# Kernel optimization log

Hardware: AMD Instinct MI355X
Metric: run time of the kernel (lower is better)

The kernel has to match this reference:

```python
import jax, jax.numpy as jnp
import numpy as np

B, C, N = 8, 512, 2048

def setup_inputs() -> dict:
    key = jax.random.key(0)
    ks = jax.random.split(key, 7)
    s = 1.0 / np.sqrt(C)
    return {
        "x": jax.random.normal(ks[0], (B, C, N), dtype=jnp.float32),
        "wq": jax.random.normal(ks[1], (C, C), dtype=jnp.float32) * s,
        "bq": jax.random.normal(ks[2], (C,), dtype=jnp.float32) * s,
        "wk": jax.random.normal(ks[3], (C, C), dtype=jnp.float32) * s,
        "bk": jax.random.normal(ks[4], (C,), dtype=jnp.float32) * s,
        "wv": jax.random.normal(ks[5], (C, C), dtype=jnp.float32) * s,
        "bv": jax.random.normal(ks[6], (C,), dtype=jnp.float32) * s,
    }

def reference(x, wq, bq, wk, bk, wv, bv):
    # Conv1d with kernel=1 == pointwise channel matmul: [B,C,N] -> [B,C,N]
    q = jnp.einsum('oc,bcn->bon', wq, x) + bq[None, :, None]
    k = jnp.einsum('oc,bcn->bon', wk, x) + bk[None, :, None]
    v = jnp.einsum('oc,bcn->bon', wv, x) + bv[None, :, None]
    # scores[b,i,j] = sum_c q[b,c,i] * k[b,c,j]; softmax over j (no scaling, as in source)
    scores = jnp.einsum('bci,bcj->bij', q, k)
    attn = jax.nn.softmax(scores, axis=-1)  # [B,N,N]
    # out[b,c,i] = sum_j v[b,c,j] * attn[b,i,j]
    out = jnp.einsum('bcj,bij->bci', v, attn)
    return out + x
```

## Files before the change

### kernel.cpp

```cpp
#include <hip/hip_runtime.h>
#include <hip/hip_bf16.h>

typedef _Float16 half_t;
typedef _Float16 f16x8 __attribute__((ext_vector_type(8)));
typedef float f32x4 __attribute__((ext_vector_type(4)));

#define AS1 __attribute__((address_space(1)))
#define AS3 __attribute__((address_space(3)))

constexpr int CB = 512;
constexpr int NB = 2048;
constexpr int BB = 8;

__device__ inline f32x4 mfma16(f16x8 a, f16x8 b, f32x4 c) {
  return __builtin_amdgcn_mfma_f32_16x16x32_f16(a, b, c, 0, 0, 0);
}

__device__ inline void xcd_swizzle(int& bx, int& by, int& bz) {
  const int gx = gridDim.x, gy = gridDim.y, gz = gridDim.z;
  const int nwg = gx * gy * gz;
  int lin = blockIdx.x + gx * (blockIdx.y + gy * blockIdx.z);
  if ((nwg & 7) == 0) {
    const int q = nwg >> 3;
    lin = (lin & 7) * q + (lin >> 3);
  }
  bx = lin % gx;
  int tmp = lin / gx;
  by = tmp % gy;
  bz = tmp / gy;
}

__global__ void prep_wu(const float* __restrict__ wv, const float* __restrict__ wk,
                        const float* __restrict__ bq,
                        half_t* __restrict__ wvh, float* __restrict__ u) {
  if (blockIdx.x < 1024) {
    int i = blockIdx.x * 256 + threadIdx.x;
    if (i < CB * CB) wvh[i] = (half_t)wv[i];
  } else {
    int d = (blockIdx.x - 1024) * 256 + threadIdx.x;
    if (d < CB) {
      float s = 0.0f;
      for (int o = 0; o < CB; o++) s += bq[o] * wk[(size_t)o * CB + d];
      u[d] = s;
    }
  }
}

__global__ __launch_bounds__(256) void compute_G_part(const float* __restrict__ wq,
                                                      const float* __restrict__ wk,
                                                      float* __restrict__ Gp) {
  __shared__ float aq[64][68];
  __shared__ float ak[64][68];
  const int c0 = blockIdx.y * 64, d0 = blockIdx.x * 64, o0 = blockIdx.z * 64;
  const int t = threadIdx.x;
  {
    const int r = t >> 2, cbase = (t & 3) * 16;
    const float* q = wq + (size_t)(o0 + r) * CB + c0 + cbase;
    const float* k = wk + (size_t)(o0 + r) * CB + d0 + cbase;
#pragma unroll
    for (int q4 = 0; q4 < 4; q4++) {
      *(float4*)&aq[r][cbase + q4 * 4] = *(const float4*)(q + q4 * 4);
      *(float4*)&ak[r][cbase + q4 * 4] = *(const float4*)(k + q4 * 4);
    }
  }
  __syncthreads();
  const int tc = t & 15, td = t >> 4;
  float acc[4][4] = {};
#pragma unroll 8
  for (int o = 0; o < 64; o++) {
    float4 a4 = *(const float4*)&aq[o][tc * 4];
    float4 b4 = *(const float4*)&ak[o][td * 4];
    float av[4] = {a4.x, a4.y, a4.z, a4.w};
    float bv[4] = {b4.x, b4.y, b4.z, b4.w};
#pragma unroll
    for (int i = 0; i < 4; i++)
#pragma unroll
      for (int j = 0; j < 4; j++)
        acc[i][j] += av[i] * bv[j];
  }
  float* gz = Gp + (size_t)blockIdx.z * CB * CB;
#pragma unroll
  for (int i = 0; i < 4; i++) {
    int c = c0 + tc * 4 + i;
#pragma unroll
    for (int j = 0; j < 4; j++)
      gz[(size_t)c * CB + d0 + td * 4 + j] = acc[i][j];
  }
}

__global__ void reduce_G(const float* __restrict__ Gp, half_t* __restrict__ Gh) {
  int i = blockIdx.x * 256 + threadIdx.x;
  if (i >= CB * CB) return;
  float s = 0.0f;
#pragma unroll
  for (int z = 0; z < 8; z++) s += Gp[(size_t)z * CB * CB + i];
  Gh[i] = (half_t)s;
}

__global__ __launch_bounds__(256) void compute_ubias(const half_t* __restrict__ xh,
                                                     const float* __restrict__ u,
                                                     float* __restrict__ ub) {
  __shared__ float us[CB];
  for (int i = threadIdx.x; i < CB; i += 256) us[i] = u[i];
  __syncthreads();
  int row = blockIdx.x * 4 + (threadIdx.x >> 6);
  int lane = threadIdx.x & 63;
  f16x8 vh = *(const f16x8*)(xh + (size_t)row * CB + lane * 8);
  float s = 0.0f;
#pragma unroll
  for (int i = 0; i < 8; i++) s += us[lane * 8 + i] * (float)vh[i];
#pragma unroll
  for (int off = 32; off; off >>= 1) s += __shfl_xor(s, off);
  if (lane == 0) ub[row] = s;
}

__global__ void transpose_x(const float* __restrict__ x, half_t* __restrict__ oh,
                            half_t* __restrict__ xn) {
  __shared__ float tile[32][33];
  int b = blockIdx.z, c0 = blockIdx.y * 32, n0 = blockIdx.x * 32;
  int tx = threadIdx.x, ty = threadIdx.y;
  const float* xb = x + (size_t)b * CB * NB;
  half_t* xnb = xn + (size_t)b * CB * NB;
#pragma unroll
  for (int r = 0; r < 4; r++) {
    float v = xb[(size_t)(c0 + ty + 8 * r) * NB + n0 + tx];
    tile[ty + 8 * r][tx] = v;
    xnb[(size_t)(c0 + ty + 8 * r) * NB + n0 + tx] = (half_t)v;
  }
  __syncthreads();
  size_t base = (size_t)b * NB * CB;
#pragma unroll
  for (int r = 0; r < 4; r++)
    oh[base + (size_t)(n0 + ty + 8 * r) * CB + c0 + tx] = (half_t)tile[tx][ty + 8 * r];
}

template <int BIAS, int EPI, int NT>
__global__ __launch_bounds__(256) void gemm_nt(
    const half_t* __restrict__ A, int lda, long sA,
    const half_t* __restrict__ Bh, int ldb, long sB,
    void* __restrict__ D, int ldd, long sD,
    const float* __restrict__ bias, long sBias,
    const half_t* __restrict__ R, int ldr, long sR) {
  constexpr int TSZ = 128 * 32;
  __shared__ alignas(16) half_t sm[3 * 2 * TSZ];

  int bxi, byi, bzi;
  xcd_swizzle(bxi, byi, bzi);
  const int t = threadIdx.x;
  const int z = bzi;
  const half_t* Ab  = A  + (size_t)z * sA + (size_t)(byi * 128) * lda;
  const half_t* Bbh = Bh + (size_t)z * sB + (size_t)(bxi * 128) * ldb;
  const int wid = t >> 6, l15 = t & 15, hi = (t >> 4) & 3;
  const int wr = wid >> 1, wc = wid & 1;
  const int lineA = t >> 2, eoff = (t & 3) * 8;

  f32x4 acc[4][4] = {};

  auto stage = [&](int buf, int kt) {
    half_t* base = sm + buf * (2 * TSZ);
#pragma unroll
    for (int p = 0; p < 2; p++) {
      size_t goA = (size_t)(p * 64 + lineA) * lda + kt * 32 + eoff;
      size_t goB = (size_t)(p * 64 + lineA) * ldb + kt * 32 + eoff;
      int lo = p * 2048 + t * 8;
      __builtin_amdgcn_global_load_lds((const AS1 void*)(Ab + goA),  (AS3 void*)(base + lo), 16, 0, 0);
      __builtin_amdgcn_global_load_lds((const AS1 void*)(Bbh + goB), (AS3 void*)(base + TSZ + lo), 16, 0, 0);
    }
  };

  stage(0, 0);
  stage(1, 1);
  asm volatile("s_waitcnt vmcnt(4)" ::: "memory");
  __builtin_amdgcn_s_barrier();
  asm volatile("" ::: "memory");

  int rb = 0;
  for (int kt = 0; kt < NT; kt++) {
    if (kt + 2 < NT) {
      int sb = rb + 2; if (sb >= 3) sb -= 3;
      stage(sb, kt + 2);
    }
    const half_t* bb = sm + rb * (2 * TSZ);
    f16x8 af[4], bf[4];
#pragma unroll
    for (int f = 0; f < 4; f++) {
      af[f] = *(const f16x8*)(bb + (wr * 64 + f * 16 + l15) * 32 + hi * 8);
      bf[f] = *(const f16x8*)(bb + TSZ + (wc * 64 + f * 16 + l15) * 32 + hi * 8);
    }
#pragma unroll
    for (int fm = 0; fm < 4; fm++)
#pragma unroll
      for (int fn = 0; fn < 4; fn++)
        acc[fm][fn] = mfma16(af[fm], bf[fn], acc[fm][fn]);

    if (kt + 1 < NT) {
      if (kt + 2 < NT) asm volatile("s_waitcnt vmcnt(4)" ::: "memory");
      else             asm volatile("s_waitcnt vmcnt(0)" ::: "memory");
      __builtin_amdgcn_s_barrier();
      asm volatile("" ::: "memory");
    }
    rb = (rb + 1 == 3) ? 0 : rb + 1;
  }

  const int row0 = byi * 128 + wr * 64;
  const int col0 = bxi * 128 + wc * 64;
#pragma unroll
  for (int fm = 0; fm < 4; fm++) {
    int rowb = row0 + fm * 16 + hi * 4;
#pragma unroll
    for (int fn = 0; fn < 4; fn++) {
      int col = col0 + fn * 16 + l15;
      float bc = (BIAS == 1) ? bias[(size_t)z * sBias + col] : 0.0f;
#pragma unroll
      for (int r = 0; r < 4; r++) {
        float val = acc[fm][fn][r] + bc;
        size_t di = (size_t)(rowb + r) * ldd + col;
        if (EPI == 3) {
          val += (float)R[(size_t)z * sR + (size_t)(rowb + r) * ldr + col];
          ((float*)D)[(size_t)z * sD + di] = val;
        } else {
          float sv = fminf(fmaxf(val * 256.0f, -32767.0f), 32767.0f);
          ((short*)D)[(size_t)z * sD + di] = (short)__float2int_rn(sv);
        }
      }
    }
  }
}

__global__ __launch_bounds__(256) void gemm_vyt(
    const half_t* __restrict__ xh, const half_t* __restrict__ wvh,
    const half_t* __restrict__ Gh, const float* __restrict__ bv,
    half_t* __restrict__ v, half_t* __restrict__ YTh) {
  constexpr int TSZ = 128 * 32;
  __shared__ alignas(16) half_t sm[2 * 2 * TSZ];

  int bxi, byi, bzi;
  xcd_swizzle(bxi, byi, bzi);
  const int t = threadIdx.x;

  const half_t* Ab;
  const half_t* Bb;
  half_t* Dz;
  int ldd, row0b, col0b;
  const float* rowbias = nullptr;
  if (bzi < 8) {
    const int z = bzi;
    Ab = wvh + (size_t)(byi * 128) * CB;
    Bb = xh + (size_t)z * NB * CB + (size_t)(bxi * 128) * CB;
    Dz = v + (size_t)z * CB * NB;
    ldd = NB; row0b = byi * 128; col0b = bxi * 128;
    rowbias = bv;
  } else {
    const int z = bzi - 8;
    const int lin2 = byi * 16 + bxi;
    const int xp = lin2 & 3, yp = lin2 >> 2;
    Ab = xh + (size_t)z * NB * CB + (size_t)(yp * 128) * CB;
    Bb = Gh + (size_t)(xp * 128) * CB;
    Dz = YTh + (size_t)z * NB * CB;
    ldd = CB; row0b = yp * 128; col0b = xp * 128;
  }

  const int wid = t >> 6, l15 = t & 15, hi = (t >> 4) & 3;
  const int wr = wid >> 1, wc = wid & 1;
  const int lineA = t >> 2, eoff = (t & 3) * 8;

  f32x4 acc[4][4] = {};

  auto stage = [&](int buf, int kt) {
    half_t* base = sm + buf * (2 * TSZ);
#pragma unroll
    for (int p = 0; p < 2; p++) {
      size_t go = (size_t)(p * 64 + lineA) * CB + kt * 32 + eoff;
      int lo = p * 2048 + t * 8;
      __builtin_amdgcn_global_load_lds((const AS1 void*)(Ab + go), (AS3 void*)(base + lo), 16, 0, 0);
      __builtin_amdgcn_global_load_lds((const AS1 void*)(Bb + go), (AS3 void*)(base + TSZ + lo), 16, 0, 0);
    }
  };

  stage(0, 0);
  __syncthreads();
  int cur = 0;
  for (int kt = 0; kt < 16; kt++) {
    if (kt + 1 < 16) stage(cur ^ 1, kt + 1);
    const half_t* bb = sm + cur * (2 * TSZ);
    f16x8 af[4], bf[4];
#pragma unroll
    for (int f = 0; f < 4; f++) {
      af[f] = *(const f16x8*)(bb + (wr * 64 + f * 16 + l15) * 32 + hi * 8);
      bf[f] = *(const f16x8*)(bb + TSZ + (wc * 64 + f * 16 + l15) * 32 + hi * 8);
    }
#pragma unroll
    for (int fm = 0; fm < 4; fm++)
#pragma unroll
      for (int fn = 0; fn < 4; fn++)
        acc[fm][fn] = mfma16(af[fm], bf[fn], acc[fm][fn]);
    __syncthreads();
    cur ^= 1;
  }

  const int row0 = row0b + wr * 64;
  const int col0 = col0b + wc * 64;
#pragma unroll
  for (int fm = 0; fm < 4; fm++) {
    int rowb = row0 + fm * 16 + hi * 4;
#pragma unroll
    for (int fn = 0; fn < 4; fn++) {
      int col = col0 + fn * 16 + l15;
#pragma unroll
      for (int r = 0; r < 4; r++) {
        float val = acc[fm][fn][r];
        if (rowbias) val += rowbias[rowb + r];
        Dz[(size_t)(rowb + r) * ldd + col] = (half_t)val;
      }
    }
  }
}

struct alignas(16) H8 { half_t h[8]; };
struct alignas(16) S8 { short s[8]; };

__global__ __launch_bounds__(256) void softmax_rows(const short* __restrict__ S,
                                                    half_t* __restrict__ P) {
  const short* row = S + (size_t)blockIdx.x * NB;
  int t = threadIdx.x;
  S8 r8 = *reinterpret_cast<const S8*>(row + t * 8);
  float vals[8];
#pragma unroll
  for (int i = 0; i < 8; i++) vals[i] = (float)r8.s[i] * 0.00390625f;
  float m = vals[0];
#pragma unroll
  for (int i = 1; i < 8; i++) m = fmaxf(m, vals[i]);
#pragma unroll
  for (int off = 32; off; off >>= 1) m = fmaxf(m, __shfl_xor(m, off));
  __shared__ float redm[4], reds[4];
  if ((t & 63) == 0) redm[t >> 6] = m;
  __syncthreads();
  m = fmaxf(fmaxf(redm[0], redm[1]), fmaxf(redm[2], redm[3]));
  float e[8], s = 0.0f;
#pragma unroll
  for (int i = 0; i < 8; i++) { e[i] = __expf(vals[i] - m); s += e[i]; }
#pragma unroll
  for (int off = 32; off; off >>= 1) s += __shfl_xor(s, off);
  if ((t & 63) == 0) reds[t >> 6] = s;
  __syncthreads();
  s = reds[0] + reds[1] + reds[2] + reds[3];
  float inv = 1.0f / s;
  H8 ob;
#pragma unroll
  for (int i = 0; i < 8; i++) ob.h[i] = (half_t)(e[i] * inv);
  *reinterpret_cast<H8*>(P + (size_t)blockIdx.x * NB + t * 8) = ob;
}

extern "C" void kernel_launch(void* const* d_in, const int* in_sizes, int n_in,
                              void* d_out, int out_size, void* d_ws, size_t ws_size,
                              hipStream_t stream) {
  const float* x  = (const float*)d_in[0];
  const float* wq = (const float*)d_in[1];
  const float* bq = (const float*)d_in[2];
  const float* wk = (const float*)d_in[3];
  const float* wv = (const float*)d_in[5];
  const float* bv = (const float*)d_in[6];
  float* out = (float*)d_out;

  const size_t MB = 1u << 20;
  if (ws_size < 196 * MB) return;

  char* ws = (char*)d_ws;
  half_t* xh   = (half_t*)(ws + 0);
  half_t* YTh  = (half_t*)(ws + 16 * MB);
  half_t* v    = (half_t*)(ws + 32 * MB);
  short*  Ss   = (short*)(ws + 48 * MB);
  float*  Gp   = (float*)(ws + 48 * MB);
  half_t* Pd   = (half_t*)(ws + 112 * MB);
  half_t* xn   = (half_t*)(ws + 176 * MB);
  half_t* Gh   = (half_t*)(ws + 192 * MB);
  half_t* wvh  = (half_t*)(ws + 192 * MB + 512 * 1024);
  float*  u    = (float*)(ws + 193 * MB);
  float*  ub   = (float*)(ws + 193 * MB + 256 * 1024);

  prep_wu<<<1026, 256, 0, stream>>>(wv, wk, bq, wvh, u);
  compute_G_part<<<dim3(8, 8, 8), 256, 0, stream>>>(wq, wk, Gp);
  reduce_G<<<1024, 256, 0, stream>>>(Gp, Gh);
  transpose_x<<<dim3(64, 16, 8), dim3(32, 8), 0, stream>>>(x, xh, xn);
  compute_ubias<<<BB * NB / 4, 256, 0, stream>>>(xh, u, ub);

  gemm_vyt<<<dim3(16, 4, 16), 256, 0, stream>>>(xh, wvh, Gh, bv, v, YTh);

  gemm_nt<1, 4, 16><<<dim3(16, 16, 8), 256, 0, stream>>>(
      xh, CB, (long)NB * CB,
      YTh, CB, (long)NB * CB,
      Ss, NB, (long)NB * NB, ub, NB, nullptr, 0, 0);

  softmax_rows<<<BB * NB, 256, 0, stream>>>(Ss, Pd);

  gemm_nt<0, 3, 64><<<dim3(16, 4, 8), 256, 0, stream>>>(
      v, NB, (long)CB * NB,
      Pd, NB, (long)NB * NB,
      out, NB, (long)CB * NB, nullptr, 0,
      xn, NB, (long)CB * NB);
}
```

Measured before the change: 209.5 us.

## Merge prep kernels into two launches and simplify gemm to double buffering

Five small preprocessing kernels (x transpose/convert, partial G, wv conversion, u, G reduction, ubias) are folded into two launches by dispatching on block index, cutting launch count and gaps between dependent kernels. Separately, the gemm_nt main loop goes from a three-stage LDS pipeline with fine-grained vmcnt waits to a two-buffer scheme with a full __syncthreads per iteration. This lowers LDS use per block, which may allow more resident blocks, but it exposes more global-load latency because only one tile is prefetched ahead and every iteration waits for all loads.

```diff
diff --git a/kernel.cpp b/kernel.cpp
--- a/kernel.cpp
+++ b/kernel.cpp
@@ -30,108 +30,116 @@
   bz = tmp / gy;
 }
 
-__global__ void prep_wu(const float* __restrict__ wv, const float* __restrict__ wk,
-                        const float* __restrict__ bq,
-                        half_t* __restrict__ wvh, float* __restrict__ u) {
-  if (blockIdx.x < 1024) {
-    int i = blockIdx.x * 256 + threadIdx.x;
-    if (i < CB * CB) wvh[i] = (half_t)wv[i];
+__global__ __launch_bounds__(256) void prep_all(
+    const float* __restrict__ x, const float* __restrict__ wq,
+    const float* __restrict__ wk, const float* __restrict__ wv,
+    const float* __restrict__ bq,
+    half_t* __restrict__ xh, half_t* __restrict__ xn,
+    half_t* __restrict__ wvh, float* __restrict__ u, float* __restrict__ Gp) {
+  __shared__ float smem[64 * 68 * 2];
+  const int b = blockIdx.x;
+  const int t = threadIdx.x;
+
+  if (b < 8192) {
+    float (*tile)[33] = (float(*)[33])smem;
+    const int bz = b >> 10, by = (b >> 6) & 15, bx = b & 63;
+    const int c0 = by * 32, n0 = bx * 32;
+    const int tx = t & 31, ty = t >> 5;
+    const float* xb = x + (size_t)bz * CB * NB;
+    half_t* xnb = xn + (size_t)bz * CB * NB;
+#pragma unroll
+    for (int r = 0; r < 4; r++) {
+      float v = xb[(size_t)(c0 + ty + 8 * r) * NB + n0 + tx];
+      tile[ty + 8 * r][tx] = v;
+      xnb[(size_t)(c0 + ty + 8 * r) * NB + n0 + tx] = (half_t)v;
+    }
+    __syncthreads();
+    size_t base = (size_t)bz * NB * CB;
+#pragma unroll
+    for (int r = 0; r < 4; r++)
+      xh[base + (size_t)(n0 + ty + 8 * r) * CB + c0 + tx] = (half_t)tile[tx][ty + 8 * r];
+  } else if (b < 8704) {
+    const int g = b - 8192;
+    const int d0 = (g & 7) * 64, c0 = ((g >> 3) & 7) * 64, o0 = (g >> 6) * 64;
+    float (*aq)[68] = (float(*)[68])smem;
+    float (*ak)[68] = (float(*)[68])(smem + 64 * 68);
+    {
+      const int r = t >> 2, cbase = (t & 3) * 16;
+      const float* q = wq + (size_t)(o0 + r) * CB + c0 + cbase;
+      const float* k = wk + (size_t)(o0 + r) * CB + d0 + cbase;
+#pragma unroll
+      for (int q4 = 0; q4 < 4; q4++) {
+        *(float4*)&aq[r][cbase + q4 * 4] = *(const float4*)(q + q4 * 4);
+        *(float4*)&ak[r][cbase + q4 * 4] = *(const float4*)(k + q4 * 4);
+      }
+    }
+    __syncthreads();
+    const int tc = t & 15, td = t >> 4;
+    float acc[4][4] = {};
+#pragma unroll 8
+    for (int o = 0; o < 64; o++) {
+      float4 a4 = *(const float4*)&aq[o][tc * 4];
+      float4 b4 = *(const float4*)&ak[o][td * 4];
+      float av[4] = {a4.x, a4.y, a4.z, a4.w};
+      float bv[4] = {b4.x, b4.y, b4.z, b4.w};
+#pragma unroll
+      for (int i = 0; i < 4; i++)
+#pragma unroll
+        for (int j = 0; j < 4; j++)
+          acc[i][j] += av[i] * bv[j];
+    }
+    float* gz = Gp + (size_t)(g >> 6) * CB * CB;
+#pragma unroll
+    for (int i = 0; i < 4; i++) {
+      int c = c0 + tc * 4 + i;
+#pragma unroll
+      for (int j = 0; j < 4; j++)
+        gz[(size_t)c * CB + d0 + td * 4 + j] = acc[i][j];
+    }
   } else {
-    int d = (blockIdx.x - 1024) * 256 + threadIdx.x;
-    if (d < CB) {
+    const int p = b - 8704;
+    if (p < 1024) {
+      int i = p * 256 + t;
+      if (i < CB * CB) wvh[i] = (half_t)wv[i];
+    } else {
+      int d = (p - 1024) * 256 + t;
+      if (d < CB) {
+        float s = 0.0f;
+        for (int o = 0; o < CB; o++) s += bq[o] * wk[(size_t)o * CB + d];
+        u[d] = s;
+      }
+    }
+  }
+}
+
+__global__ __launch_bounds__(256) void prep2(
+    const float* __restrict__ Gp, half_t* __restrict__ Gh,
+    const half_t* __restrict__ xh, const float* __restrict__ u,
+    float* __restrict__ ub) {
+  const int b = blockIdx.x;
+  const int t = threadIdx.x;
+  if (b < 1024) {
+    int i = b * 256 + t;
+    if (i < CB * CB) {
       float s = 0.0f;
-      for (int o = 0; o < CB; o++) s += bq[o] * wk[(size_t)o * CB + d];
-      u[d] = s;
-    }
-  }
-}
-
-__global__ __launch_bounds__(256) void compute_G_part(const float* __restrict__ wq,
-                                                      const float* __restrict__ wk,
-                                                      float* __restrict__ Gp) {
-  __shared__ float aq[64][68];
-  __shared__ float ak[64][68];
-  const int c0 = blockIdx.y * 64, d0 = blockIdx.x * 64, o0 = blockIdx.z * 64;
-  const int t = threadIdx.x;
-  {
-    const int r = t >> 2, cbase = (t & 3) * 16;
-    const float* q = wq + (size_t)(o0 + r) * CB + c0 + cbase;
-    const float* k = wk + (size_t)(o0 + r) * CB + d0 + cbase;
-#pragma unroll
-    for (int q4 = 0; q4 < 4; q4++) {
-      *(float4*)&aq[r][cbase + q4 * 4] = *(const float4*)(q + q4 * 4);
-      *(float4*)&ak[r][cbase + q4 * 4] = *(const float4*)(k + q4 * 4);
-    }
-  }
-  __syncthreads();
-  const int tc = t & 15, td = t >> 4;
-  float acc[4][4] = {};
-#pragma unroll 8
-  for (int o = 0; o < 64; o++) {
-    float4 a4 = *(const float4*)&aq[o][tc * 4];
-    float4 b4 = *(const float4*)&ak[o][td * 4];
-    float av[4] = {a4.x, a4.y, a4.z, a4.w};
-    float bv[4] = {b4.x, b4.y, b4.z, b4.w};
-#pragma unroll
-    for (int i = 0; i < 4; i++)
-#pragma unroll
-      for (int j = 0; j < 4; j++)
-        acc[i][j] += av[i] * bv[j];
-  }
-  float* gz = Gp + (size_t)blockIdx.z * CB * CB;
-#pragma unroll
-  for (int i = 0; i < 4; i++) {
-    int c = c0 + tc * 4 + i;
-#pragma unroll
-    for (int j = 0; j < 4; j++)
-      gz[(size_t)c * CB + d0 + td * 4 + j] = acc[i][j];
-  }
-}
-
-__global__ void reduce_G(const float* __restrict__ Gp, half_t* __restrict__ Gh) {
-  int i = blockIdx.x * 256 + threadIdx.x;
-  if (i >= CB * CB) return;
-  float s = 0.0f;
-#pragma unroll
-  for (int z = 0; z < 8; z++) s += Gp[(size_t)z * CB * CB + i];
-  Gh[i] = (half_t)s;
-}
-
-__global__ __launch_bounds__(256) void compute_ubias(const half_t* __restrict__ xh,
-                                                     const float* __restrict__ u,
-                                                     float* __restrict__ ub) {
-  __shared__ float us[CB];
-  for (int i = threadIdx.x; i < CB; i += 256) us[i] = u[i];
-  __syncthreads();
-  int row = blockIdx.x * 4 + (threadIdx.x >> 6);
-  int lane = threadIdx.x & 63;
-  f16x8 vh = *(const f16x8*)(xh + (size_t)row * CB + lane * 8);
-  float s = 0.0f;
-#pragma unroll
-  for (int i = 0; i < 8; i++) s += us[lane * 8 + i] * (float)vh[i];
-#pragma unroll
-  for (int off = 32; off; off >>= 1) s += __shfl_xor(s, off);
-  if (lane == 0) ub[row] = s;
-}
-
-__global__ void transpose_x(const float* __restrict__ x, half_t* __restrict__ oh,
-                            half_t* __restrict__ xn) {
-  __shared__ float tile[32][33];
-  int b = blockIdx.z, c0 = blockIdx.y * 32, n0 = blockIdx.x * 32;
-  int tx = threadIdx.x, ty = threadIdx.y;
-  const float* xb = x + (size_t)b * CB * NB;
-  half_t* xnb = xn + (size_t)b * CB * NB;
-#pragma unroll
-  for (int r = 0; r < 4; r++) {
-    float v = xb[(size_t)(c0 + ty + 8 * r) * NB + n0 + tx];
-    tile[ty + 8 * r][tx] = v;
-    xnb[(size_t)(c0 + ty + 8 * r) * NB + n0 + tx] = (half_t)v;
-  }
-  __syncthreads();
-  size_t base = (size_t)b * NB * CB;
-#pragma unroll
-  for (int r = 0; r < 4; r++)
-    oh[base + (size_t)(n0 + ty + 8 * r) * CB + c0 + tx] = (half_t)tile[tx][ty + 8 * r];
+#pragma unroll
+      for (int z = 0; z < 8; z++) s += Gp[(size_t)z * CB * CB + i];
+      Gh[i] = (half_t)s;
+    }
+  } else {
+    __shared__ float us[CB];
+    for (int i = t; i < CB; i += 256) us[i] = u[i];
+    __syncthreads();
+    int row = (b - 1024) * 4 + (t >> 6);
+    int lane = t & 63;
+    f16x8 vh = *(const f16x8*)(xh + (size_t)row * CB + lane * 8);
+    float s = 0.0f;
+#pragma unroll
+    for (int i = 0; i < 8; i++) s += us[lane * 8 + i] * (float)vh[i];
+#pragma unroll
+    for (int off = 32; off; off >>= 1) s += __shfl_xor(s, off);
+    if (lane == 0) ub[row] = s;
+  }
 }
 
 template <int BIAS, int EPI, int NT>
@@ -142,7 +150,7 @@
     const float* __restrict__ bias, long sBias,
     const half_t* __restrict__ R, int ldr, long sR) {
   constexpr int TSZ = 128 * 32;
-  __shared__ alignas(16) half_t sm[3 * 2 * TSZ];
+  __shared__ alignas(16) half_t sm[2 * 2 * TSZ];
 
   int bxi, byi, bzi;
   xcd_swizzle(bxi, byi, bzi);
@@ -169,18 +177,11 @@
   };
 
   stage(0, 0);
-  stage(1, 1);
-  asm volatile("s_waitcnt vmcnt(4)" ::: "memory");
-  __builtin_amdgcn_s_barrier();
-  asm volatile("" ::: "memory");
-
-  int rb = 0;
+  __syncthreads();
+  int cur = 0;
   for (int kt = 0; kt < NT; kt++) {
-    if (kt + 2 < NT) {
-      int sb = rb + 2; if (sb >= 3) sb -= 3;
-      stage(sb, kt + 2);
-    }
-    const half_t* bb = sm + rb * (2 * TSZ);
+    if (kt + 1 < NT) stage(cur ^ 1, kt + 1);
+    const half_t* bb = sm + cur * (2 * TSZ);
     f16x8 af[4], bf[4];
 #pragma unroll
     for (int f = 0; f < 4; f++) {
@@ -192,14 +193,8 @@
 #pragma unroll
       for (int fn = 0; fn < 4; fn++)
         acc[fm][fn] = mfma16(af[fm], bf[fn], acc[fm][fn]);
-
-    if (kt + 1 < NT) {
-      if (kt + 2 < NT) asm volatile("s_waitcnt vmcnt(4)" ::: "memory");
-      else             asm volatile("s_waitcnt vmcnt(0)" ::: "memory");
-      __builtin_amdgcn_s_barrier();
-      asm volatile("" ::: "memory");
-    }
-    rb = (rb + 1 == 3) ? 0 : rb + 1;
+    __syncthreads();
+    cur ^= 1;
   }
 
   const int row0 = byi * 128 + wr * 64;
@@ -378,11 +373,9 @@
   float*  u    = (float*)(ws + 193 * MB);
   float*  ub   = (float*)(ws + 193 * MB + 256 * 1024);
 
-  prep_wu<<<1026, 256, 0, stream>>>(wv, wk, bq, wvh, u);
-  compute_G_part<<<dim3(8, 8, 8), 256, 0, stream>>>(wq, wk, Gp);
-  reduce_G<<<1024, 256, 0, stream>>>(Gp, Gh);
-  transpose_x<<<dim3(64, 16, 8), dim3(32, 8), 0, stream>>>(x, xh, xn);
-  compute_ubias<<<BB * NB / 4, 256, 0, stream>>>(xh, u, ub);
+  prep_all<<<9730, 256, 0, stream>>>(x, wq, wk, wv, bq, xh, xn, wvh, u, Gp);
+
+  prep2<<<5120, 256, 0, stream>>>(Gp, Gh, xh, u, ub);
 
   gemm_vyt<<<dim3(16, 4, 16), 256, 0, stream>>>(xh, wvh, Gh, bv, v, YTh);
 
```

Measured after the change: 201.8 us. 3.7% less time.
